# Kernel optimization log

Hardware: AMD Instinct MI355X
Metric: run time of the kernel (lower is better)

The kernel has to match this reference:

```python
import jax, jax.numpy as jnp
import numpy as np

# Sizes (see init_kwargs / shape_source)
N = 65536      # total points
B = 8          # batch elements
PPB = N // B   # points per batch element (8192, divisible by WS -> no padding)
D = 256        # d_model
H = 8          # nhead
DH = D // H
L = 4          # num_layers
FF = 2048      # torch TransformerEncoderLayer default dim_feedforward
RES = 128      # resolution (coordinate range / embedding table size)
BITS = 7       # ceil(log2(RES)); higher bits of morton loop are zero
WS = 128       # window_size
EPS = 1e-5     # LayerNorm eps


def setup_inputs() -> dict:
    key = jax.random.key(0)
    ks = jax.random.split(key, 16)
    s = 0.02
    batch_col = (jnp.arange(N) // PPB).astype(jnp.int32)
    xyz = jax.random.randint(ks[0], (N, 3), 0, RES, dtype=jnp.int32)
    coords = jnp.concatenate([batch_col[:, None], xyz], axis=1)
    features = jax.random.normal(ks[1], (N, D), jnp.float32)
    inp = {
        'coords': coords,
        'features': features,
        # learned positional embedding tables
        'pe_x': jax.random.normal(ks[2], (RES, D), jnp.float32) * s,
        'pe_y': jax.random.normal(ks[3], (RES, D), jnp.float32) * s,
        'pe_z': jax.random.normal(ks[4], (RES, D), jnp.float32) * s,
        'pe_s': jax.random.normal(ks[5], (RES, D), jnp.float32) * s,
        # stacked transformer encoder layer params (torch post-norm layer)
        'Wqkv': jax.random.normal(ks[6], (L, 3 * D, D), jnp.float32) * s,
        'bqkv': jnp.zeros((L, 3 * D), jnp.float32),
        'Wo': jax.random.normal(ks[7], (L, D, D), jnp.float32) * s,
        'bo': jnp.zeros((L, D), jnp.float32),
        'W1': jax.random.normal(ks[8], (L, FF, D), jnp.float32) * s,
        'b1': jnp.zeros((L, FF), jnp.float32),
        'W2': jax.random.normal(ks[9], (L, D, FF), jnp.float32) * s,
        'b2': jnp.zeros((L, D), jnp.float32),
        'g1': jnp.ones((L, D), jnp.float32),
        'be1': jnp.zeros((L, D), jnp.float32),
        'g2': jnp.ones((L, D), jnp.float32),
        'be2': jnp.zeros((L, D), jnp.float32),
    }
    return inp


def _morton_key(coords):
    # interleave bits of x,y,z (z lowest), prefix with batch index so batch order is preserved
    x, y, z = coords[:, 1], coords[:, 2], coords[:, 3]
    m = jnp.zeros_like(x)
    for i in range(BITS):
        m = m | (((x >> i) & 1) << (3 * i + 2)) \
              | (((y >> i) & 1) << (3 * i + 1)) \
              | (((z >> i) & 1) << (3 * i))
    return coords[:, 0] * (1 << (3 * BITS)) + m


def _ln(x, g, b):
    mu = jnp.mean(x, axis=-1, keepdims=True)
    var = jnp.mean(jnp.square(x - mu), axis=-1, keepdims=True)
    return (x - mu) * jax.lax.rsqrt(var + EPS) * g + b


def _encoder(x, params):
    # x: [Wn, WS, D]; torch TransformerEncoderLayer, post-norm, relu, no dropout (eval)
    scale = float(DH) ** -0.5

    def layer(h, p):
        Wqkv, bqkv, Wo, bo, W1, b1, W2, b2, g1, be1, g2, be2 = p
        Wn = h.shape[0]
        qkv = h @ Wqkv.T + bqkv                      # [Wn, WS, 3D]
        q, k, v = jnp.split(qkv, 3, axis=-1)
        q = q.reshape(Wn, WS, H, DH)
        k = k.reshape(Wn, WS, H, DH)
        v = v.reshape(Wn, WS, H, DH)
        att = jax.nn.softmax(jnp.einsum('wqhd,wkhd->whqk', q, k) * scale, axis=-1)
        o = jnp.einsum('whqk,wkhd->wqhd', att, v).reshape(Wn, WS, D) @ Wo.T + bo
        h = _ln(h + o, g1, be1)
        ff = jax.nn.relu(h @ W1.T + b1) @ W2.T + b2
        h = _ln(h + ff, g2, be2)
        return h, None

    x, _ = jax.lax.scan(layer, x, params)
    return x


def reference(coords, features, pe_x, pe_y, pe_z, pe_s,
              Wqkv, bqkv, Wo, bo, W1, b1, W2, b2, g1, be1, g2, be2):
    # 1) Morton sort (stable, batch-major)
    idx = jnp.argsort(_morton_key(coords))
    sc = coords[idx]
    sf = features[idx]
    # 2) learned positional encoding (stride = 1)
    pe = pe_x[sc[:, 1]] + pe_y[sc[:, 2]] + pe_z[sc[:, 3]] + pe_s[1]
    x = sf + pe
    # 3) window split: PPB % WS == 0, interval == 1 -> exact tiling, no padding
    x = x.reshape(-1, WS, D)                          # [Wn, WS, D]
    # 4) transformer encoder over windows
    x = _encoder(x, (Wqkv, bqkv, Wo, bo, W1, b1, W2, b2, g1, be1, g2, be2))
    # 5) gather back (all masks True -> simple reshape); output in sorted order
    return x.reshape(N, D)
```

## Files before the change

### kernel.cpp

```cpp
#include <hip/hip_runtime.h>

typedef unsigned int u32;
typedef unsigned short u16;

#define NPTS 65536
#define DMODEL 256
#define NHEAD 8
#define DHEAD 32
#define NLAYER 4
#define FFDIM 2048
#define WSIZE 128
#define LNEPS 1e-5f
#define RG 256

#define KSTR 36
#define VSTR 132
#define PSTR 132

typedef __attribute__((ext_vector_type(8))) short short8;
typedef __attribute__((ext_vector_type(4))) float floatx4;

__device__ __forceinline__ float bf2f(u16 v) {
    u32 u = ((u32)v) << 16;
    float f;
    __builtin_memcpy(&f, &u, 4);
    return f;
}
__device__ __forceinline__ u16 f2bf(float f) {
    u32 u;
    __builtin_memcpy(&u, &f, 4);
    u32 r = (u + 0x7fffu + ((u >> 16) & 1u)) >> 16;
    return (u16)r;
}

__device__ __forceinline__ void gl_lds16(const void* g, void* l) {
    __builtin_amdgcn_global_load_lds((const __attribute__((address_space(1))) u32*)g,
                                     (__attribute__((address_space(3))) u32*)l, 16, 0, 0);
}

__global__ __launch_bounds__(256) void morton_kernel(const int* __restrict__ coords,
                                                     u32* __restrict__ key, u32* __restrict__ val,
                                                     u32* __restrict__ ghist) {
    __shared__ u32 hh[256];
    int tid = threadIdx.x;
    hh[tid] = 0;
    int i = blockIdx.x * 256 + tid;
    int b = coords[4 * i + 0];
    int x = coords[4 * i + 1];
    int y = coords[4 * i + 2];
    int z = coords[4 * i + 3];
    u32 m = 0;
#pragma unroll
    for (int t = 0; t < 7; ++t) {
        m |= ((u32)((x >> t) & 1) << (3 * t + 2)) | ((u32)((y >> t) & 1) << (3 * t + 1)) |
             ((u32)((z >> t) & 1) << (3 * t));
    }
    u32 k = ((u32)b << 21) | m;
    key[i] = k;
    val[i] = (u32)i;
    __syncthreads();
    atomicAdd(&hh[k & 255u], 1u);
    __syncthreads();
    ghist[(size_t)tid * RG + blockIdx.x] = hh[tid];
}

__global__ __launch_bounds__(256) void hist_kernel(const u32* __restrict__ key, u32* __restrict__ ghist,
                                                   int shift) {
    __shared__ u32 h[256];
    int tid = threadIdx.x;
    h[tid] = 0;
    __syncthreads();
    u32 k = key[blockIdx.x * 256 + tid];
    atomicAdd(&h[(k >> shift) & 255u], 1u);
    __syncthreads();
    ghist[(size_t)tid * RG + blockIdx.x] = h[tid];
}

__global__ __launch_bounds__(256) void scan_up(u32* __restrict__ g, u32* __restrict__ aux) {
    __shared__ u32 wsum[4];
    int tid = threadIdx.x;
    int lane = tid & 63;
    int wave = tid >> 6;
    size_t base = (size_t)blockIdx.x * 1024 + (size_t)tid * 4;
    uint4 v = *(const uint4*)(g + base);
    u32 s = v.x + v.y + v.z + v.w;
    u32 inc = s;
#pragma unroll
    for (int off = 1; off < 64; off <<= 1) {
        u32 u = __shfl_up(inc, off, 64);
        if (lane >= off) inc += u;
    }
    if (lane == 63) wsum[wave] = inc;
    __syncthreads();
    u32 woff = 0;
    for (int w = 0; w < wave; ++w) woff += wsum[w];
    u32 excl = woff + inc - s;
    uint4 o;
    o.x = excl;
    o.y = excl + v.x;
    o.z = excl + v.x + v.y;
    o.w = excl + v.x + v.y + v.z;
    *(uint4*)(g + base) = o;
    if (tid == 255) aux[blockIdx.x] = woff + inc;
}

__global__ __launch_bounds__(256) void scatter_kernel(const u32* __restrict__ keyin, const u32* __restrict__ valin,
                                                      u32* __restrict__ keyout, u32* __restrict__ valout,
                                                      const u32* __restrict__ ghist, const u32* __restrict__ aux,
                                                      int shift) {
    __shared__ u32 whist[4][256];
    __shared__ u32 apre[64];
    int tid = threadIdx.x;
    int lane = tid & 63;
    int wave = tid >> 6;
    uint4 z = {0u, 0u, 0u, 0u};
    ((uint4*)&whist[0][0])[tid] = z;
    if (tid < 64) {
        u32 a = aux[tid];
        u32 inc = a;
#pragma unroll
        for (int off = 1; off < 64; off <<= 1) {
            u32 u = __shfl_up(inc, off, 64);
            if (lane >= off) inc += u;
        }
        apre[tid] = inc - a;
    }
    int gi = blockIdx.x * 256 + tid;
    u32 k = keyin[gi];
    u32 v = valin[gi];
    u32 b = (k >> shift) & 255u;
    __syncthreads();
    unsigned long long m = ~0ull;
#pragma unroll
    for (int bit = 0; bit < 8; ++bit) {
        unsigned long long bb = __ballot((int)((b >> bit) & 1u));
        m &= ((b >> bit) & 1u) ? bb : ~bb;
    }
    unsigned long long below = (lane == 0) ? 0ull : (m & ((1ull << lane) - 1ull));
    int rlane = __popcll(below);
    int cnt = __popcll(m);
    if (rlane == 0) whist[wave][b] = (u32)cnt;
    __syncthreads();
    u32 rank = (u32)rlane;
    for (int w = 0; w < wave; ++w) rank += whist[w][b];
    u32 e = b * (u32)RG + blockIdx.x;
    u32 dst = ghist[e] + apre[e >> 10] + rank;
    keyout[dst] = k;
    valout[dst] = v;
}

__global__ __launch_bounds__(256) void cvt_all_kernel(const float* __restrict__ s1, u16* __restrict__ d1, int n1,
                                                      const float* __restrict__ s2, u16* __restrict__ d2, int n2,
                                                      const float* __restrict__ s3, u16* __restrict__ d3, int n3,
                                                      const float* __restrict__ s4, u16* __restrict__ d4, int n4) {
    int i = blockIdx.x * 256 + threadIdx.x;
    if (i < n1) { d1[i] = f2bf(s1[i]); return; }
    i -= n1;
    if (i < n2) { d2[i] = f2bf(s2[i]); return; }
    i -= n2;
    if (i < n3) { d3[i] = f2bf(s3[i]); return; }
    i -= n3;
    if (i < n4) {
        int l = i >> 19;
        int rem = i & 524287;
        int o = rem >> 11;
        int k = rem & 2047;
        int out = (l << 19) + ((k >> 10) << 18) + (o << 10) + (k & 1023);
        d4[out] = f2bf(s4[i]);
    }
}

template <bool HF32>
__global__ __launch_bounds__(256) void gather_pe_kernel(const u32* __restrict__ idx, const int* __restrict__ coords,
                                                        const float* __restrict__ feat,
                                                        const float* __restrict__ pex, const float* __restrict__ pey,
                                                        const float* __restrict__ pez, const float* __restrict__ pes,
                                                        float* __restrict__ h, u16* __restrict__ xb) {
    int row = blockIdx.x * 4 + (threadIdx.x >> 6);
    int lane = threadIdx.x & 63;
    int src = (int)idx[row];
    int cx = coords[4 * src + 1];
    int cy = coords[4 * src + 2];
    int cz = coords[4 * src + 3];
    int c = lane * 4;
    float4 f = *(const float4*)(feat + (size_t)src * DMODEL + c);
    float4 px = *(const float4*)(pex + (size_t)cx * DMODEL + c);
    float4 py = *(const float4*)(pey + (size_t)cy * DMODEL + c);
    float4 pz = *(const float4*)(pez + (size_t)cz * DMODEL + c);
    float4 ps = *(const float4*)(pes + (size_t)1 * DMODEL + c);
    float4 r;
    r.x = f.x + px.x + py.x + pz.x + ps.x;
    r.y = f.y + px.y + py.y + pz.y + ps.y;
    r.z = f.z + px.z + py.z + pz.z + ps.z;
    r.w = f.w + px.w + py.w + pz.w + ps.w;
    if (HF32) *(float4*)(h + (size_t)row * DMODEL + c) = r;
    ushort4 o;
    o.x = f2bf(r.x);
    o.y = f2bf(r.y);
    o.z = f2bf(r.z);
    o.w = f2bf(r.w);
    *(ushort4*)(xb + (size_t)row * DMODEL + c) = o;
}

template <bool RELU, bool BF16OUT, bool ACCUM>
__global__ __launch_bounds__(256, 5) void gemm_bt(const u16* __restrict__ A, const u16* __restrict__ W,
                                                  const float* __restrict__ bias, void* __restrict__ Cout,
                                                  int M, int O, int K) {
    __shared__ __align__(16) u16 lA[2 * 128 * 32];
    __shared__ __align__(16) u16 lB[2 * 128 * 32];
    const int tid = threadIdx.x;
    const int lane = tid & 63;
    const int wave = tid >> 6;
    const int wr = wave >> 1;
    const int wc = wave & 1;
    const int quad = lane >> 4;
    const int l16 = lane & 15;
    const size_t row0 = (size_t)blockIdx.x * 128;
    const size_t col0 = (size_t)blockIdx.y * 128;
    floatx4 acc[4][4] = {};

    const int r0 = tid >> 2;
    const int sg0 = (tid & 3) ^ ((r0 >> 1) & 3);
    const u16* pA = A + (row0 + r0) * (size_t)K + (sg0 << 3);
    const u16* pW = W + (col0 + r0) * (size_t)K + (sg0 << 3);
    const size_t rstep = (size_t)64 * K;
    const int oA = tid * 8;

    const int nt = K >> 5;
    gl_lds16(pA, lA + oA);
    gl_lds16(pA + rstep, lA + oA + 2048);
    gl_lds16(pW, lB + oA);
    gl_lds16(pW + rstep, lB + oA + 2048);
    pA += 32;
    pW += 32;

    const int sx = (quad ^ ((l16 >> 1) & 3)) << 3;
    const int rdA = (wr * 64 + l16) * 32 + sx;
    const int rdB = (wc * 64 + l16) * 32 + sx;
    int buf = 0;
    for (int t = 0; t < nt; ++t) {
        if (t + 1 < nt) {
            const int nb = (buf ^ 1) * 4096;
            gl_lds16(pA, lA + nb + oA);
            gl_lds16(pA + rstep, lA + nb + oA + 2048);
            gl_lds16(pW, lB + nb + oA);
            gl_lds16(pW + rstep, lB + nb + oA + 2048);
            pA += 32;
            pW += 32;
            asm volatile("s_waitcnt vmcnt(4)" ::: "memory");
        } else {
            asm volatile("s_waitcnt vmcnt(0)" ::: "memory");
        }
        __builtin_amdgcn_s_barrier();
        const u16* la = lA + buf * 4096 + rdA;
        const u16* lb = lB + buf * 4096 + rdB;
        short8 af[4], bf[4];
#pragma unroll
        for (int r = 0; r < 4; ++r) af[r] = *(const short8*)(la + r * 512);
#pragma unroll
        for (int c = 0; c < 4; ++c) bf[c] = *(const short8*)(lb + c * 512);
#pragma unroll
        for (int r = 0; r < 4; ++r)
#pragma unroll
            for (int c = 0; c < 4; ++c)
                acc[r][c] = __builtin_amdgcn_mfma_f32_16x16x32_bf16(af[r], bf[c], acc[r][c], 0, 0, 0);
        if (t + 1 < nt) __builtin_amdgcn_s_barrier();
        buf ^= 1;
    }

#pragma unroll
    for (int r = 0; r < 4; ++r) {
#pragma unroll
        for (int c = 0; c < 4; ++c) {
            size_t col = col0 + wc * 64 + c * 16 + l16;
            float bv = bias ? bias[col] : 0.f;
#pragma unroll
            for (int reg = 0; reg < 4; ++reg) {
                size_t row = row0 + wr * 64 + r * 16 + quad * 4 + reg;
                float v = acc[r][c][reg] + bv;
                if (RELU) v = fmaxf(v, 0.f);
                if (BF16OUT) {
                    ((u16*)Cout)[row * O + col] = f2bf(v);
                } else {
                    float* p = (float*)Cout + row * O + col;
                    if (ACCUM) v += *p;
                    *p = v;
                }
            }
        }
    }
}

__global__ __launch_bounds__(256, 2) void gemm_w1(const u16* __restrict__ A, const u16* __restrict__ W,
                                                  const float* __restrict__ bias, u16* __restrict__ Cout,
                                                  int O, int K) {
    __shared__ __align__(16) u16 lA[2 * 128 * 32];
    __shared__ __align__(16) u16 lB[2 * 256 * 32];
    const int tid = threadIdx.x;
    const int lane = tid & 63;
    const int wave = tid >> 6;
    const int wr = wave >> 1;
    const int wc = wave & 1;
    const int quad = lane >> 4;
    const int l16 = lane & 15;
    const size_t row0 = (size_t)blockIdx.x * 128;
    const size_t col0 = (size_t)blockIdx.y * 256;
    floatx4 acc[4][8] = {};

    const int r0 = tid >> 2;
    const int sg0 = (tid & 3) ^ ((r0 >> 1) & 3);
    const u16* pA = A + (row0 + r0) * (size_t)K + (sg0 << 3);
    const u16* pW = W + (col0 + r0) * (size_t)K + (sg0 << 3);
    const size_t rstep = (size_t)64 * K;
    const int oA = tid * 8;

    const int nt = K >> 5;
    gl_lds16(pA, lA + oA);
    gl_lds16(pA + rstep, lA + oA + 2048);
    gl_lds16(pW, lB + oA);
    gl_lds16(pW + rstep, lB + oA + 2048);
    gl_lds16(pW + 2 * rstep, lB + oA + 4096);
    gl_lds16(pW + 3 * rstep, lB + oA + 6144);
    pA += 32;
    pW += 32;

    const int sx = (quad ^ ((l16 >> 1) & 3)) << 3;
    const int rdA = (wr * 64 + l16) * 32 + sx;
    const int rdB = (wc * 128 + l16) * 32 + sx;
    int buf = 0;
    for (int t = 0; t < nt; ++t) {
        if (t + 1 < nt) {
            const int na = (buf ^ 1) * 4096;
            const int nb = (buf ^ 1) * 8192;
            gl_lds16(pA, lA + na + oA);
            gl_lds16(pA + rstep, lA + na + oA + 2048);
            gl_lds16(pW, lB + nb + oA);
            gl_lds16(pW + rstep, lB + nb + oA + 2048);
            gl_lds16(pW + 2 * rstep, lB + nb + oA + 4096);
            gl_lds16(pW + 3 * rstep, lB + nb + oA + 6144);
            pA += 32;
            pW += 32;
            asm volatile("s_waitcnt vmcnt(6)" ::: "memory");
        } else {
            asm volatile("s_waitcnt vmcnt(0)" ::: "memory");
        }
        __builtin_amdgcn_s_barrier();
        const u16* la = lA + buf * 4096 + rdA;
        const u16* lb = lB + buf * 8192 + rdB;
        short8 af[4], bf[8];
#pragma unroll
        for (int r = 0; r < 4; ++r) af[r] = *(const short8*)(la + r * 512);
#pragma unroll
        for (int c = 0; c < 8; ++c) bf[c] = *(const short8*)(lb + c * 512);
#pragma unroll
        for (int r = 0; r < 4; ++r)
#pragma unroll
            for (int c = 0; c < 8; ++c)
                acc[r][c] = __builtin_amdgcn_mfma_f32_16x16x32_bf16(af[r], bf[c], acc[r][c], 0, 0, 0);
        if (t + 1 < nt) __builtin_amdgcn_s_barrier();
        buf ^= 1;
    }

#pragma unroll
    for (int r = 0; r < 4; ++r) {
#pragma unroll
        for (int c = 0; c < 8; ++c) {
            size_t col = col0 + wc * 128 + c * 16 + l16;
            float bv = bias[col];
#pragma unroll
            for (int reg = 0; reg < 4; ++reg) {
                size_t row = row0 + wr * 64 + r * 16 + quad * 4 + reg;
                float v = fmaxf(acc[r][c][reg] + bv, 0.f);
                Cout[row * O + col] = f2bf(v);
            }
        }
    }
}

__global__ __launch_bounds__(128) void attn_kernel(const u16* __restrict__ qkv, u16* __restrict__ outb) {
    const int wh = blockIdx.x;
    const int w = wh >> 3;
    const int h = wh & 7;
    const int tid = threadIdx.x;
    const int wave = tid >> 6;
    const int lane = tid & 63;
    const int quad = lane >> 4;
    const int l16 = lane & 15;
    __shared__ __align__(16) u16 lK[128 * KSTR];
    __shared__ __align__(16) u16 lVt[32 * VSTR];
    __shared__ __align__(16) u16 lP[128 * PSTR];
    const u16* base = qkv + (size_t)w * WSIZE * (3 * DMODEL);

    {
        const u16* krow = base + (size_t)tid * (3 * DMODEL) + DMODEL + h * DHEAD;
        const u16* vrow = base + (size_t)tid * (3 * DMODEL) + 2 * DMODEL + h * DHEAD;
#pragma unroll
        for (int p = 0; p < 4; ++p)
            *(short8*)&lK[tid * KSTR + p * 8] = *(const short8*)(krow + p * 8);
        u16 varr[32];
#pragma unroll
        for (int p = 0; p < 4; ++p)
            *(short8*)&varr[p * 8] = *(const short8*)(vrow + p * 8);
#pragma unroll
        for (int d = 0; d < DHEAD; ++d) lVt[d * VSTR + tid] = varr[d];
    }
    short8 af[4];
#pragma unroll
    for (int mi = 0; mi < 4; ++mi)
        af[mi] = *(const short8*)(base + (size_t)(wave * 64 + mi * 16 + l16) * (3 * DMODEL) + h * DHEAD + quad * 8);
    __syncthreads();

    floatx4 acc[4][8] = {};
#pragma unroll
    for (int ni = 0; ni < 8; ++ni) {
        short8 bk = *(const short8*)&lK[(ni * 16 + l16) * KSTR + quad * 8];
#pragma unroll
        for (int mi = 0; mi < 4; ++mi)
            acc[mi][ni] = __builtin_amdgcn_mfma_f32_16x16x32_bf16(af[mi], bk, acc[mi][ni], 0, 0, 0);
    }

    const float scale = 0.17677669529663687f;
    float inv[4][4];
#pragma unroll
    for (int mi = 0; mi < 4; ++mi) {
#pragma unroll
        for (int reg = 0; reg < 4; ++reg) {
            float m = acc[mi][0][reg];
#pragma unroll
            for (int ni = 1; ni < 8; ++ni) m = fmaxf(m, acc[mi][ni][reg]);
            m = fmaxf(m, __shfl_xor(m, 1, 64));
            m = fmaxf(m, __shfl_xor(m, 2, 64));
            m = fmaxf(m, __shfl_xor(m, 4, 64));
            m = fmaxf(m, __shfl_xor(m, 8, 64));
            float e[8];
            float sum = 0.f;
#pragma unroll
            for (int ni = 0; ni < 8; ++ni) {
                e[ni] = __expf((acc[mi][ni][reg] - m) * scale);
                sum += e[ni];
            }
            sum += __shfl_xor(sum, 1, 64);
            sum += __shfl_xor(sum, 2, 64);
            sum += __shfl_xor(sum, 4, 64);
            sum += __shfl_xor(sum, 8, 64);
            inv[mi][reg] = 1.f / sum;
            int row = wave * 64 + mi * 16 + quad * 4 + reg;
#pragma unroll
            for (int ni = 0; ni < 8; ++ni) lP[row * PSTR + ni * 16 + l16] = f2bf(e[ni]);
        }
    }

    floatx4 acc2[4][2] = {};
#pragma unroll
    for (int kt = 0; kt < 4; ++kt) {
        short8 pa[4];
#pragma unroll
        for (int mi = 0; mi < 4; ++mi)
            pa[mi] = *(const short8*)&lP[(wave * 64 + mi * 16 + l16) * PSTR + kt * 32 + quad * 8];
#pragma unroll
        for (int c = 0; c < 2; ++c) {
            short8 bv = *(const short8*)&lVt[(c * 16 + l16) * VSTR + kt * 32 + quad * 8];
#pragma unroll
            for (int mi = 0; mi < 4; ++mi)
                acc2[mi][c] = __builtin_amdgcn_mfma_f32_16x16x32_bf16(pa[mi], bv, acc2[mi][c], 0, 0, 0);
        }
    }

#pragma unroll
    for (int mi = 0; mi < 4; ++mi) {
#pragma unroll
        for (int c = 0; c < 2; ++c) {
#pragma unroll
            for (int reg = 0; reg < 4; ++reg) {
                int row = wave * 64 + mi * 16 + quad * 4 + reg;
                outb[(size_t)(w * WSIZE + row) * DMODEL + h * DHEAD + c * 16 + l16] =
                    f2bf(acc2[mi][c][reg] * inv[mi][reg]);
            }
        }
    }
}

template <bool HF32, bool OUTF32>
__global__ __launch_bounds__(256) void resid_ln_kernel(const void* __restrict__ hin, const float* __restrict__ delta,
                                                       const float* __restrict__ g, const float* __restrict__ b,
                                                       float* __restrict__ hout, void* __restrict__ nout) {
    int row = blockIdx.x * 4 + (threadIdx.x >> 6);
    int lane = threadIdx.x & 63;
    int c = lane * 4;
    float4 x;
    if (HF32) {
        x = *(const float4*)((const float*)hin + (size_t)row * DMODEL + c);
    } else {
        ushort4 hv = *(const ushort4*)((const u16*)hin + (size_t)row * DMODEL + c);
        x.x = bf2f(hv.x);
        x.y = bf2f(hv.y);
        x.z = bf2f(hv.z);
        x.w = bf2f(hv.w);
    }
    float4 d = *(const float4*)(delta + (size_t)row * DMODEL + c);
    x.x += d.x;
    x.y += d.y;
    x.z += d.z;
    x.w += d.w;
    float s = x.x + x.y + x.z + x.w;
#pragma unroll
    for (int off = 32; off > 0; off >>= 1) s += __shfl_xor(s, off, 64);
    float mu = s * (1.f / 256.f);
    float d0 = x.x - mu, d1 = x.y - mu, d2 = x.z - mu, d3 = x.w - mu;
    float vs = d0 * d0 + d1 * d1 + d2 * d2 + d3 * d3;
#pragma unroll
    for (int off = 32; off > 0; off >>= 1) vs += __shfl_xor(vs, off, 64);
    float rs = rsqrtf(vs * (1.f / 256.f) + LNEPS);
    float4 gg = *(const float4*)(g + c);
    float4 bb = *(const float4*)(b + c);
    float4 y;
    y.x = d0 * rs * gg.x + bb.x;
    y.y = d1 * rs * gg.y + bb.y;
    y.z = d2 * rs * gg.z + bb.z;
    y.w = d3 * rs * gg.w + bb.w;
    if (HF32) *(float4*)(hout + (size_t)row * DMODEL + c) = y;
    if (OUTF32) {
        *(float4*)((float*)nout + (size_t)row * DMODEL + c) = y;
    } else {
        ushort4 o;
        o.x = f2bf(y.x);
        o.y = f2bf(y.y);
        o.z = f2bf(y.z);
        o.w = f2bf(y.w);
        *(ushort4*)((u16*)nout + (size_t)row * DMODEL + c) = o;
    }
}

extern "C" void kernel_launch(void* const* d_in, const int* in_sizes, int n_in,
                              void* d_out, int out_size, void* d_ws, size_t ws_size,
                              hipStream_t stream) {
    (void)in_sizes;
    (void)n_in;
    (void)out_size;
    const int* coords = (const int*)d_in[0];
    const float* feat = (const float*)d_in[1];
    const float* pex = (const float*)d_in[2];
    const float* pey = (const float*)d_in[3];
    const float* pez = (const float*)d_in[4];
    const float* pes = (const float*)d_in[5];
    const float* Wqkv = (const float*)d_in[6];
    const float* bqkv = (const float*)d_in[7];
    const float* Wo = (const float*)d_in[8];
    const float* bo = (const float*)d_in[9];
    const float* W1 = (const float*)d_in[10];
    const float* b1 = (const float*)d_in[11];
    const float* W2 = (const float*)d_in[12];
    const float* b2 = (const float*)d_in[13];
    const float* g1 = (const float*)d_in[14];
    const float* be1 = (const float*)d_in[15];
    const float* g2 = (const float*)d_in[16];
    const float* be2 = (const float*)d_in[17];

    auto al = [](size_t x) { return (x + 255) & ~(size_t)255; };
    const size_t sortB = 4 * al((size_t)NPTS * 4) + al((size_t)256 * RG * 4) + 256;
    const size_t wqkvB = al((size_t)NLAYER * 3 * DMODEL * DMODEL * 2);
    const size_t woB = al((size_t)NLAYER * DMODEL * DMODEL * 2);
    const size_t w1B = al((size_t)NLAYER * FFDIM * DMODEL * 2);
    const size_t w2B = al((size_t)NLAYER * DMODEL * FFDIM * 2);
    const size_t wB = wqkvB + woB + w1B + w2B;
    const size_t xbB = al((size_t)NPTS * DMODEL * 2);
    const size_t hB = al((size_t)NPTS * DMODEL * 4);

    int CH = 0;
    bool modeA = true;
    for (int ch = 65536; ch >= 256 && !CH; ch >>= 1) {
        size_t need = sortB + wB + xbB + hB + al((size_t)ch * 2048) + al((size_t)ch * 1024) + 65536;
        if (need <= ws_size) { CH = ch; modeA = true; }
    }
    if (!CH) {
        for (int ch = 65536; ch >= 256 && !CH; ch >>= 1) {
            size_t need = sortB + wB + xbB + al((size_t)ch * 2048) + al((size_t)ch * 1024) + 65536;
            if (need <= ws_size) { CH = ch; modeA = false; }
        }
    }
    if (!CH) { CH = 256; modeA = false; }

    char* ws = (char*)d_ws;
    size_t off = 0;
    auto alloc = [&](size_t bytes) -> void* {
        void* p = ws + off;
        off += al(bytes);
        return p;
    };
    u32* key0 = (u32*)alloc(NPTS * 4);
    u32* val0 = (u32*)alloc(NPTS * 4);
    u32* key1 = (u32*)alloc(NPTS * 4);
    u32* val1 = (u32*)alloc(NPTS * 4);
    u32* ghist = (u32*)alloc(256 * RG * 4);
    u32* aux = (u32*)alloc(64 * 4);
    u16* wqkv_b = (u16*)alloc((size_t)NLAYER * 3 * DMODEL * DMODEL * 2);
    u16* wo_b = (u16*)alloc((size_t)NLAYER * DMODEL * DMODEL * 2);
    u16* w1_b = (u16*)alloc((size_t)NLAYER * FFDIM * DMODEL * 2);
    u16* w2_b = (u16*)alloc((size_t)NLAYER * DMODEL * FFDIM * 2);
    u16* xb = (u16*)alloc((size_t)NPTS * DMODEL * 2);
    float* h = modeA ? (float*)alloc((size_t)NPTS * DMODEL * 4) : nullptr;
    u16* scratch1 = (u16*)alloc((size_t)CH * 2048);
    float* tmpc = (float*)alloc((size_t)CH * 1024);

    morton_kernel<<<NPTS / 256, 256, 0, stream>>>(coords, key0, val0, ghist);

    u32 *ki = key0, *vi = val0, *ko = key1, *vo = val1;
    for (int p = 0; p < 3; ++p) {
        if (p > 0) hist_kernel<<<RG, 256, 0, stream>>>(ki, ghist, p * 8);
        scan_up<<<64, 256, 0, stream>>>(ghist, aux);
        scatter_kernel<<<RG, 256, 0, stream>>>(ki, vi, ko, vo, ghist, aux, p * 8);
        u32* t;
        t = ki; ki = ko; ko = t;
        t = vi; vi = vo; vo = t;
    }
    const u32* idx = vi;

    {
        const int n1 = NLAYER * 3 * DMODEL * DMODEL;
        const int n2 = NLAYER * DMODEL * DMODEL;
        const int n3 = NLAYER * FFDIM * DMODEL;
        const int n4 = NLAYER * DMODEL * FFDIM;
        cvt_all_kernel<<<(n1 + n2 + n3 + n4) / 256, 256, 0, stream>>>(Wqkv, wqkv_b, n1, Wo, wo_b, n2,
                                                                      W1, w1_b, n3, W2, w2_b, n4);
    }

    if (modeA)
        gather_pe_kernel<true><<<NPTS / 4, 256, 0, stream>>>(idx, coords, feat, pex, pey, pez, pes, h, xb);
    else
        gather_pe_kernel<false><<<NPTS / 4, 256, 0, stream>>>(idx, coords, feat, pex, pey, pez, pes, nullptr, xb);

    const int nch = NPTS / CH;
    u16* qkvc = scratch1;
    u16* attoutc = scratch1 + (size_t)CH * 768;
    u16* midc = scratch1;
    for (int l = 0; l < NLAYER; ++l) {
        for (int c = 0; c < nch; ++c) {
            u16* xc = xb + (size_t)c * CH * DMODEL;
            float* hc = modeA ? h + (size_t)c * CH * DMODEL : nullptr;
            gemm_bt<false, true, false><<<dim3(CH / 128, 6), 256, 0, stream>>>(
                xc, wqkv_b + (size_t)l * 3 * DMODEL * DMODEL, bqkv + (size_t)l * 3 * DMODEL, qkvc,
                CH, 3 * DMODEL, DMODEL);
            attn_kernel<<<(CH / WSIZE) * NHEAD, 128, 0, stream>>>(qkvc, attoutc);
            gemm_bt<false, false, false><<<dim3(CH / 128, 2), 256, 0, stream>>>(
                attoutc, wo_b + (size_t)l * DMODEL * DMODEL, bo + (size_t)l * DMODEL, tmpc,
                CH, DMODEL, DMODEL);
            if (modeA)
                resid_ln_kernel<true, false><<<CH / 4, 256, 0, stream>>>(hc, tmpc, g1 + (size_t)l * DMODEL,
                                                                         be1 + (size_t)l * DMODEL, hc, xc);
            else
                resid_ln_kernel<false, false><<<CH / 4, 256, 0, stream>>>(xc, tmpc, g1 + (size_t)l * DMODEL,
                                                                          be1 + (size_t)l * DMODEL, nullptr, xc);
            for (int j = 0; j < 2; ++j) {
                gemm_w1<<<dim3(CH / 128, 4), 256, 0, stream>>>(
                    xc, w1_b + (size_t)l * FFDIM * DMODEL + (size_t)j * 1024 * DMODEL,
                    b1 + (size_t)l * FFDIM + j * 1024, midc, 1024, DMODEL);
                if (j == 0)
                    gemm_bt<false, false, false><<<dim3(CH / 128, 2), 256, 0, stream>>>(
                        midc, w2_b + (size_t)l * 524288, b2 + (size_t)l * DMODEL, tmpc, CH, DMODEL, 1024);
                else
                    gemm_bt<false, false, true><<<dim3(CH / 128, 2), 256, 0, stream>>>(
                        midc, w2_b + (size_t)l * 524288 + 262144, nullptr, tmpc, CH, DMODEL, 1024);
            }
            bool last = (l == NLAYER - 1);
            void* outc = last ? (void*)((float*)d_out + (size_t)c * CH * DMODEL) : (void*)xc;
            if (modeA) {
                if (last)
                    resid_ln_kernel<true, true><<<CH / 4, 256, 0, stream>>>(hc, tmpc, g2 + (size_t)l * DMODEL,
                                                                            be2 + (size_t)l * DMODEL, hc, outc);
                else
                    resid_ln_kernel<true, false><<<CH / 4, 256, 0, stream>>>(hc, tmpc, g2 + (size_t)l * DMODEL,
                                                                             be2 + (size_t)l * DMODEL, hc, outc);
            } else {
                if (last)
                    resid_ln_kernel<false, true><<<CH / 4, 256, 0, stream>>>(xc, tmpc, g2 + (size_t)l * DMODEL,
                                                                             be2 + (size_t)l * DMODEL, nullptr, outc);
                else
                    resid_ln_kernel<false, false><<<CH / 4, 256, 0, stream>>>(xc, tmpc, g2 + (size_t)l * DMODEL,
                                                                              be2 + (size_t)l * DMODEL, nullptr, outc);
            }
        }
    }
}
```

Measured before the change: 2.280 ms.

## Keep attention probabilities in registers and split FFN by rows

```diff
diff --git a/kernel.cpp b/kernel.cpp
--- a/kernel.cpp
+++ b/kernel.cpp
@@ -15,9 +15,9 @@
 
 #define KSTR 36
 #define VSTR 132
-#define PSTR 132
 
 typedef __attribute__((ext_vector_type(8))) short short8;
+typedef __attribute__((ext_vector_type(4))) short short4v;
 typedef __attribute__((ext_vector_type(4))) float floatx4;
 
 __device__ __forceinline__ float bf2f(u16 v) {
@@ -160,14 +160,7 @@
     i -= n2;
     if (i < n3) { d3[i] = f2bf(s3[i]); return; }
     i -= n3;
-    if (i < n4) {
-        int l = i >> 19;
-        int rem = i & 524287;
-        int o = rem >> 11;
-        int k = rem & 2047;
-        int out = (l << 19) + ((k >> 10) << 18) + (o << 10) + (k & 1023);
-        d4[out] = f2bf(s4[i]);
-    }
+    if (i < n4) d4[i] = f2bf(s4[i]);
 }
 
 template <bool HF32>
@@ -202,7 +195,7 @@
     *(ushort4*)(xb + (size_t)row * DMODEL + c) = o;
 }
 
-template <bool RELU, bool BF16OUT, bool ACCUM>
+template <bool RELU, bool BF16OUT>
 __global__ __launch_bounds__(256, 5) void gemm_bt(const u16* __restrict__ A, const u16* __restrict__ W,
                                                   const float* __restrict__ bias, void* __restrict__ Cout,
                                                   int M, int O, int K) {
@@ -273,19 +266,16 @@
 #pragma unroll
         for (int c = 0; c < 4; ++c) {
             size_t col = col0 + wc * 64 + c * 16 + l16;
-            float bv = bias ? bias[col] : 0.f;
+            float bv = bias[col];
 #pragma unroll
             for (int reg = 0; reg < 4; ++reg) {
                 size_t row = row0 + wr * 64 + r * 16 + quad * 4 + reg;
                 float v = acc[r][c][reg] + bv;
                 if (RELU) v = fmaxf(v, 0.f);
-                if (BF16OUT) {
+                if (BF16OUT)
                     ((u16*)Cout)[row * O + col] = f2bf(v);
-                } else {
-                    float* p = (float*)Cout + row * O + col;
-                    if (ACCUM) v += *p;
-                    *p = v;
-                }
+                else
+                    ((float*)Cout)[row * O + col] = v;
             }
         }
     }
@@ -377,7 +367,7 @@
     }
 }
 
-__global__ __launch_bounds__(128) void attn_kernel(const u16* __restrict__ qkv, u16* __restrict__ outb) {
+__global__ __launch_bounds__(128, 2) void attn_kernel(const u16* __restrict__ qkv, u16* __restrict__ outb) {
     const int wh = blockIdx.x;
     const int w = wh >> 3;
     const int h = wh & 7;
@@ -388,7 +378,6 @@
     const int l16 = lane & 15;
     __shared__ __align__(16) u16 lK[128 * KSTR];
     __shared__ __align__(16) u16 lVt[32 * VSTR];
-    __shared__ __align__(16) u16 lP[128 * PSTR];
     const u16* base = qkv + (size_t)w * WSIZE * (3 * DMODEL);
 
     {
@@ -404,78 +393,76 @@
 #pragma unroll
         for (int d = 0; d < DHEAD; ++d) lVt[d * VSTR + tid] = varr[d];
     }
-    short8 af[4];
-#pragma unroll
-    for (int mi = 0; mi < 4; ++mi)
-        af[mi] = *(const short8*)(base + (size_t)(wave * 64 + mi * 16 + l16) * (3 * DMODEL) + h * DHEAD + quad * 8);
-    __syncthreads();
-
-    floatx4 acc[4][8] = {};
-#pragma unroll
-    for (int ni = 0; ni < 8; ++ni) {
-        short8 bk = *(const short8*)&lK[(ni * 16 + l16) * KSTR + quad * 8];
-#pragma unroll
-        for (int mi = 0; mi < 4; ++mi)
-            acc[mi][ni] = __builtin_amdgcn_mfma_f32_16x16x32_bf16(af[mi], bk, acc[mi][ni], 0, 0, 0);
+    short8 aq[4];
+#pragma unroll
+    for (int qi = 0; qi < 4; ++qi)
+        aq[qi] = *(const short8*)(base + (size_t)(wave * 64 + qi * 16 + l16) * (3 * DMODEL) + h * DHEAD + quad * 8);
+    __syncthreads();
+
+    floatx4 acc[8][4] = {};
+#pragma unroll
+    for (int ki = 0; ki < 8; ++ki) {
+        short8 ak = *(const short8*)&lK[(ki * 16 + l16) * KSTR + quad * 8];
+#pragma unroll
+        for (int qi = 0; qi < 4; ++qi)
+            acc[ki][qi] = __builtin_amdgcn_mfma_f32_16x16x32_bf16(ak, aq[qi], acc[ki][qi], 0, 0, 0);
     }
 
     const float scale = 0.17677669529663687f;
-    float inv[4][4];
-#pragma unroll
-    for (int mi = 0; mi < 4; ++mi) {
-#pragma unroll
-        for (int reg = 0; reg < 4; ++reg) {
-            float m = acc[mi][0][reg];
-#pragma unroll
-            for (int ni = 1; ni < 8; ++ni) m = fmaxf(m, acc[mi][ni][reg]);
-            m = fmaxf(m, __shfl_xor(m, 1, 64));
-            m = fmaxf(m, __shfl_xor(m, 2, 64));
-            m = fmaxf(m, __shfl_xor(m, 4, 64));
-            m = fmaxf(m, __shfl_xor(m, 8, 64));
-            float e[8];
-            float sum = 0.f;
-#pragma unroll
-            for (int ni = 0; ni < 8; ++ni) {
-                e[ni] = __expf((acc[mi][ni][reg] - m) * scale);
-                sum += e[ni];
-            }
-            sum += __shfl_xor(sum, 1, 64);
-            sum += __shfl_xor(sum, 2, 64);
-            sum += __shfl_xor(sum, 4, 64);
-            sum += __shfl_xor(sum, 8, 64);
-            inv[mi][reg] = 1.f / sum;
-            int row = wave * 64 + mi * 16 + quad * 4 + reg;
-#pragma unroll
-            for (int ni = 0; ni < 8; ++ni) lP[row * PSTR + ni * 16 + l16] = f2bf(e[ni]);
-        }
-    }
-
-    floatx4 acc2[4][2] = {};
-#pragma unroll
-    for (int kt = 0; kt < 4; ++kt) {
-        short8 pa[4];
-#pragma unroll
-        for (int mi = 0; mi < 4; ++mi)
-            pa[mi] = *(const short8*)&lP[(wave * 64 + mi * 16 + l16) * PSTR + kt * 32 + quad * 8];
-#pragma unroll
-        for (int c = 0; c < 2; ++c) {
-            short8 bv = *(const short8*)&lVt[(c * 16 + l16) * VSTR + kt * 32 + quad * 8];
-#pragma unroll
-            for (int mi = 0; mi < 4; ++mi)
-                acc2[mi][c] = __builtin_amdgcn_mfma_f32_16x16x32_bf16(pa[mi], bv, acc2[mi][c], 0, 0, 0);
-        }
-    }
-
-#pragma unroll
-    for (int mi = 0; mi < 4; ++mi) {
-#pragma unroll
-        for (int c = 0; c < 2; ++c) {
-#pragma unroll
-            for (int reg = 0; reg < 4; ++reg) {
-                int row = wave * 64 + mi * 16 + quad * 4 + reg;
-                outb[(size_t)(w * WSIZE + row) * DMODEL + h * DHEAD + c * 16 + l16] =
-                    f2bf(acc2[mi][c][reg] * inv[mi][reg]);
-            }
+    float inv[4];
+    short4v pb[8][4];
+#pragma unroll
+    for (int qi = 0; qi < 4; ++qi) {
+        float m = acc[0][qi][0];
+#pragma unroll
+        for (int ki = 0; ki < 8; ++ki)
+#pragma unroll
+            for (int reg = 0; reg < 4; ++reg) m = fmaxf(m, acc[ki][qi][reg]);
+        m = fmaxf(m, __shfl_xor(m, 16, 64));
+        m = fmaxf(m, __shfl_xor(m, 32, 64));
+        float sum = 0.f;
+#pragma unroll
+        for (int ki = 0; ki < 8; ++ki) {
+            float e0 = __expf((acc[ki][qi][0] - m) * scale);
+            float e1 = __expf((acc[ki][qi][1] - m) * scale);
+            float e2 = __expf((acc[ki][qi][2] - m) * scale);
+            float e3 = __expf((acc[ki][qi][3] - m) * scale);
+            sum += e0 + e1 + e2 + e3;
+            short4v pv;
+            pv[0] = (short)f2bf(e0);
+            pv[1] = (short)f2bf(e1);
+            pv[2] = (short)f2bf(e2);
+            pv[3] = (short)f2bf(e3);
+            pb[ki][qi] = pv;
+        }
+        sum += __shfl_xor(sum, 16, 64);
+        sum += __shfl_xor(sum, 32, 64);
+        inv[qi] = 1.f / sum;
+    }
+
+    floatx4 o[2][4] = {};
+#pragma unroll
+    for (int ki = 0; ki < 8; ++ki) {
+        short4v av0 = *(const short4v*)&lVt[(size_t)l16 * VSTR + ki * 16 + quad * 4];
+        short4v av1 = *(const short4v*)&lVt[(size_t)(16 + l16) * VSTR + ki * 16 + quad * 4];
+#pragma unroll
+        for (int qi = 0; qi < 4; ++qi) {
+            o[0][qi] = __builtin_amdgcn_mfma_f32_16x16x16bf16_1k(av0, pb[ki][qi], o[0][qi], 0, 0, 0);
+            o[1][qi] = __builtin_amdgcn_mfma_f32_16x16x16bf16_1k(av1, pb[ki][qi], o[1][qi], 0, 0, 0);
+        }
+    }
+
+#pragma unroll
+    for (int half = 0; half < 2; ++half) {
+#pragma unroll
+        for (int qi = 0; qi < 4; ++qi) {
+            int q = wave * 64 + qi * 16 + l16;
+            ushort4 ov;
+            ov.x = f2bf(o[half][qi][0] * inv[qi]);
+            ov.y = f2bf(o[half][qi][1] * inv[qi]);
+            ov.z = f2bf(o[half][qi][2] * inv[qi]);
+            ov.w = f2bf(o[half][qi][3] * inv[qi]);
+            *(ushort4*)&outb[(size_t)(w * WSIZE + q) * DMODEL + h * DHEAD + half * 16 + quad * 4] = ov;
         }
     }
 }
@@ -637,11 +624,11 @@
         for (int c = 0; c < nch; ++c) {
             u16* xc = xb + (size_t)c * CH * DMODEL;
             float* hc = modeA ? h + (size_t)c * CH * DMODEL : nullptr;
-            gemm_bt<false, true, false><<<dim3(CH / 128, 6), 256, 0, stream>>>(
+            gemm_bt<false, true><<<dim3(CH / 128, 6), 256, 0, stream>>>(
                 xc, wqkv_b + (size_t)l * 3 * DMODEL * DMODEL, bqkv + (size_t)l * 3 * DMODEL, qkvc,
                 CH, 3 * DMODEL, DMODEL);
             attn_kernel<<<(CH / WSIZE) * NHEAD, 128, 0, stream>>>(qkvc, attoutc);
-            gemm_bt<false, false, false><<<dim3(CH / 128, 2), 256, 0, stream>>>(
+            gemm_bt<false, false><<<dim3(CH / 128, 2), 256, 0, stream>>>(
                 attoutc, wo_b + (size_t)l * DMODEL * DMODEL, bo + (size_t)l * DMODEL, tmpc,
                 CH, DMODEL, DMODEL);
             if (modeA)
@@ -650,16 +637,14 @@
             else
                 resid_ln_kernel<false, false><<<CH / 4, 256, 0, stream>>>(xc, tmpc, g1 + (size_t)l * DMODEL,
                                                                           be1 + (size_t)l * DMODEL, nullptr, xc);
-            for (int j = 0; j < 2; ++j) {
-                gemm_w1<<<dim3(CH / 128, 4), 256, 0, stream>>>(
-                    xc, w1_b + (size_t)l * FFDIM * DMODEL + (size_t)j * 1024 * DMODEL,
-                    b1 + (size_t)l * FFDIM + j * 1024, midc, 1024, DMODEL);
-                if (j == 0)
-                    gemm_bt<false, false, false><<<dim3(CH / 128, 2), 256, 0, stream>>>(
-                        midc, w2_b + (size_t)l * 524288, b2 + (size_t)l * DMODEL, tmpc, CH, DMODEL, 1024);
-                else
-                    gemm_bt<false, false, true><<<dim3(CH / 128, 2), 256, 0, stream>>>(
-                        midc, w2_b + (size_t)l * 524288 + 262144, nullptr, tmpc, CH, DMODEL, 1024);
+            const int MH = CH / 2;
+            for (int hf = 0; hf < 2; ++hf) {
+                const u16* xh = xc + (size_t)hf * MH * DMODEL;
+                gemm_w1<<<dim3(MH / 128, FFDIM / 256), 256, 0, stream>>>(
+                    xh, w1_b + (size_t)l * FFDIM * DMODEL, b1 + (size_t)l * FFDIM, midc, FFDIM, DMODEL);
+                gemm_bt<false, false><<<dim3(MH / 128, DMODEL / 128), 256, 0, stream>>>(
+                    midc, w2_b + (size_t)l * DMODEL * FFDIM, b2 + (size_t)l * DMODEL,
+                    tmpc + (size_t)hf * MH * DMODEL, MH, DMODEL, FFDIM);
             }
             bool last = (l == NLAYER - 1);
             void* outc = last ? (void*)((float*)d_out + (size_t)c * CH * DMODEL) : (void*)xc;
```

Result: faster. 2.220 ms (-2.6%).
